# Optimization experiments

Hardware: AMD Instinct MI355X
Metric: run time of the kernel (lower is better)

## Reference

```python
import jax, jax.numpy as jnp
import numpy as np

N_HEADS = 16
DIM = 1024
HEAD_DIM = DIM // N_HEADS

def setup_inputs() -> dict:
    key = jax.random.key(0)
    ks = jax.random.split(key, 5)
    x = jax.random.normal(ks[0], (4, 2048, DIM), dtype=jnp.float32)
    W_attn = jax.random.normal(ks[1], (DIM, 3 * DIM), dtype=jnp.float32) / np.sqrt(DIM)
    b_attn = jnp.zeros((3 * DIM,), dtype=jnp.float32)
    W_proj = jax.random.normal(ks[2], (DIM, DIM), dtype=jnp.float32) / np.sqrt(DIM)
    b_proj = jnp.zeros((DIM,), dtype=jnp.float32)
    return {"x": x, "W_attn": W_attn, "b_attn": b_attn, "W_proj": W_proj, "b_proj": b_proj}

def reference(x, W_attn, b_attn, W_proj, b_proj):
    B, S, D = x.shape
    qkv = x @ W_attn + b_attn                      # [B,S,3D]
    q, k, v = jnp.split(qkv, 3, axis=2)
    def heads(t):
        return t.reshape(B, S, N_HEADS, HEAD_DIM).transpose(0, 2, 1, 3)  # [B,H,S,hd]
    qh, kh, vh = heads(q), heads(k), heads(v)
    scale = 1.0 / np.sqrt(HEAD_DIM).astype(np.float32)
    scores = jnp.einsum('bhqd,bhkd->bhqk', qh, kh) * scale  # [B,H,S,S]
    causal = jnp.tril(jnp.ones((S, S), dtype=bool))
    scores = jnp.where(causal, scores, -jnp.inf)
    probs = jax.nn.softmax(scores, axis=-1)
    ctx = jnp.einsum('bhqk,bhkd->bhqd', probs, vh)           # [B,H,S,hd]
    ctx = ctx.transpose(0, 2, 1, 3).reshape(B, S, D)
    return ctx @ W_proj + b_proj
```

## Files before the change

kernel.cpp:

```cpp
#include <hip/hip_runtime.h>
#include <hip/hip_bf16.h>
#include <stdint.h>

typedef __attribute__((ext_vector_type(4))) float  f32x4a;
typedef __attribute__((ext_vector_type(8))) short  bf16x8s;
typedef __attribute__((ext_vector_type(8))) unsigned short u16x8;

#define QSCALE 0.18033688011112042f

static __device__ __forceinline__ unsigned short f2bf(float f) {
    union { float f; uint32_t u; } v; v.f = f;
    uint32_t u = v.u;
    return (unsigned short)((u + 0x7FFFu + ((u >> 16) & 1u)) >> 16);
}

static __device__ __forceinline__ unsigned int pack2bf(float lo, float hi) {
    __hip_bfloat162 t = __float22bfloat162_rn(make_float2(lo, hi));
    union { __hip_bfloat162 b; unsigned int u; } c; c.b = t;
    return c.u;
}

static __device__ __forceinline__ float exp2a(float x) {
    float r;
    asm("v_exp_f32 %0, %1" : "=v"(r) : "v"(x));
    return r;
}

#define GLL(src, dst)                                                          \
    __builtin_amdgcn_global_load_lds(                                          \
        (const __attribute__((address_space(1))) void*)(src),                  \
        (__attribute__((address_space(3))) void*)(dst), 16, 0, 0)

__global__ __launch_bounds__(256) void k_cvt_bf16(const float* __restrict__ in,
                                                  unsigned short* __restrict__ out, int n8) {
    int i = blockIdx.x * blockDim.x + threadIdx.x;
    if (i >= n8) return;
    const float4* p = (const float4*)(in + (size_t)i * 8);
    float4 a = p[0], b = p[1];
    u16x8 o;
    o[0] = f2bf(a.x); o[1] = f2bf(a.y); o[2] = f2bf(a.z); o[3] = f2bf(a.w);
    o[4] = f2bf(b.x); o[5] = f2bf(b.y); o[6] = f2bf(b.z); o[7] = f2bf(b.w);
    *(u16x8*)(out + (size_t)i * 8) = o;
}

__global__ __launch_bounds__(256) void k_scale_bias(const float* __restrict__ b,
                                                    float* __restrict__ out,
                                                    int n, int nscale, float sc) {
    int i = blockIdx.x * blockDim.x + threadIdx.x;
    if (i >= n) return;
    out[i] = b[i] * (i < nscale ? sc : 1.0f);
}

__global__ __launch_bounds__(256) void k_transpose_w(const float* __restrict__ W,
                                                     unsigned short* __restrict__ Wt,
                                                     int K, int N, float sc, int nscale) {
    __shared__ float tile[64][68];
    int bx = blockIdx.x;
    int ntn = N >> 6;
    int kt = bx / ntn, nt = bx % ntn;
    int t = threadIdx.x;
    int r0 = t >> 4;
    int c4 = (t & 15) << 2;
    for (int i = 0; i < 4; ++i) {
        int k = r0 + i * 16;
        float4 v = *(const float4*)(W + (size_t)(kt * 64 + k) * N + nt * 64 + c4);
        tile[k][c4 + 0] = v.x; tile[k][c4 + 1] = v.y;
        tile[k][c4 + 2] = v.z; tile[k][c4 + 3] = v.w;
    }
    __syncthreads();
    int nl = t >> 2;
    int kc = (t & 3) << 4;
    float s = (nt * 64 + nl < nscale) ? sc : 1.0f;
    unsigned short* dst = Wt + (size_t)(nt * 64 + nl) * K + kt * 64 + kc;
    u16x8 o0, o1;
    for (int i = 0; i < 8; ++i) o0[i] = f2bf(tile[kc + i][nl] * s);
    for (int i = 0; i < 8; ++i) o1[i] = f2bf(tile[kc + 8 + i][nl] * s);
    *(u16x8*)dst = o0;
    *(u16x8*)(dst + 8) = o1;
}

template<int OUT_BF16, int VW>
__global__ __launch_bounds__(512, 4) void k_gemm2b(const unsigned short* __restrict__ A,
                                                   const unsigned short* __restrict__ Bt,
                                                   const float* __restrict__ bias,
                                                   void* __restrict__ Cout,
                                                   unsigned short* __restrict__ vt,
                                                   int M, int N, int K, int ntn) {
    __shared__ __align__(16) unsigned short S[3][12288];
    unsigned short* Sf = &S[0][0];

    int nwg = gridDim.x;
    int bid = blockIdx.x;
    int wg = (bid & 7) * (nwg >> 3) + (bid >> 3);
    int mt = wg / ntn, nt = wg % ntn;
    size_t m0 = (size_t)mt * 128, n0 = (size_t)nt * 256;

    int tid = threadIdx.x;
    int w = tid >> 6, lane = tid & 63;
    int wm = w >> 2, wn = w & 3;
    int l15 = lane & 15, l4 = lane >> 4;

    int srow = tid >> 2;
    int sch = (tid & 3) ^ ((srow >> 1) & 3);
    const unsigned short* Asrc = A  + (m0 + srow) * (size_t)K + sch * 8;
    const unsigned short* Bsrc = Bt + (n0 + srow) * (size_t)K + sch * 8;

#define STG(bufoff, kt)                                                                   \
    do {                                                                                  \
        GLL(Asrc + (size_t)(kt) * 32,                    Sf + (bufoff) + tid * 8);        \
        GLL(Bsrc + (size_t)(kt) * 32,                    Sf + (bufoff) + 4096 + tid * 8); \
        GLL(Bsrc + (size_t)(kt) * 32 + (size_t)128 * K,  Sf + (bufoff) + 8192 + tid * 8); \
    } while (0)

    int ck = (l4 ^ ((l15 >> 1) & 3)) * 8;
    int aoff = (wm * 64 + l15) * 32 + ck;
    int boff = 4096 + (wn * 64 + l15) * 32 + ck;

    f32x4a acc[4][4] = {};

#define BAR() __builtin_amdgcn_s_barrier()

    int NT = K >> 5;

    STG(0, 0);
    STG(12288, 1);
    asm volatile("s_waitcnt vmcnt(3)" ::: "memory");
    __builtin_amdgcn_sched_barrier(0);
    BAR();

    int cb = 0;
    for (int t = 0; t < NT; ++t) {
        int sb = cb + 24576; if (sb >= 36864) sb -= 36864;
        bool more = (t + 2) < NT;
        if (more) STG(sb, t + 2);
        bf16x8s af[4], bf[4];
        #pragma unroll
        for (int q = 0; q < 4; ++q) af[q] = *(const bf16x8s*)(Sf + cb + aoff + q * 512);
        #pragma unroll
        for (int q = 0; q < 4; ++q) bf[q] = *(const bf16x8s*)(Sf + cb + boff + q * 512);
        __builtin_amdgcn_s_setprio(1);
        #pragma unroll
        for (int mf = 0; mf < 4; ++mf)
            #pragma unroll
            for (int nf = 0; nf < 4; ++nf)
                acc[mf][nf] = __builtin_amdgcn_mfma_f32_16x16x32_bf16(af[mf], bf[nf],
                                                                      acc[mf][nf], 0, 0, 0);
        __builtin_amdgcn_s_setprio(0);
        if (more) { asm volatile("s_waitcnt vmcnt(3)" ::: "memory"); }
        else      { asm volatile("s_waitcnt vmcnt(0)" ::: "memory"); }
        __builtin_amdgcn_sched_barrier(0);
        BAR();
        cb += 12288; if (cb >= 36864) cb = 0;
    }

    if (VW && nt >= 8) {
        int b = (int)(m0 >> 11);
        int sb_ = ((int)m0 & 2047) + wm * 64;
        #pragma unroll
        for (int nf = 0; nf < 4; ++nf) {
            int vc = ((int)n0 - 2048) + wn * 64 + nf * 16 + l15;
            int h = vc >> 6, d = vc & 63;
            float bv = bias[2048 + vc];
            unsigned short* vrow = vt + ((size_t)(b * 16 + h) * 64 + d) * 2048;
            #pragma unroll
            for (int mf = 0; mf < 4; ++mf) {
                int s = sb_ + mf * 16 + l4 * 4;
                uint2 pv = make_uint2(pack2bf(acc[mf][nf][0] + bv, acc[mf][nf][1] + bv),
                                      pack2bf(acc[mf][nf][2] + bv, acc[mf][nf][3] + bv));
                *(uint2*)(vrow + s) = pv;
            }
        }
    } else {
        #pragma unroll
        for (int nf = 0; nf < 4; ++nf) {
            int col = (int)n0 + wn * 64 + nf * 16 + l15;
            float bv = bias[col];
            #pragma unroll
            for (int mf = 0; mf < 4; ++mf) {
                int rbase = (int)m0 + wm * 64 + mf * 16 + l4 * 4;
                #pragma unroll
                for (int rr = 0; rr < 4; ++rr) {
                    float v = acc[mf][nf][rr] + bv;
                    if (OUT_BF16)
                        ((unsigned short*)Cout)[(size_t)(rbase + rr) * N + col] = f2bf(v);
                    else
                        ((float*)Cout)[(size_t)(rbase + rr) * N + col] = v;
                }
            }
        }
    }
#undef STG
#undef BAR
}

__global__ __launch_bounds__(256, 2) void k_attn(const unsigned short* __restrict__ qkv,
                                                 const unsigned short* __restrict__ vt,
                                                 unsigned short* __restrict__ ctx) {
    __shared__ unsigned short Ks[3][4096];
    __shared__ unsigned short Vs[3][4096];
    __shared__ unsigned short Pb[4][2048];
    int bx = blockIdx.x;
    int bh = bx & 63;
    int pr = bx >> 6;
    int b = bh >> 4, hd = bh & 15;
    int tid = threadIdx.x;
    int w = tid >> 6, lane = tid & 63;
    int l15 = lane & 15, l4 = lane >> 4;

    const unsigned short* Qb  = qkv + (size_t)b * 2048 * 3072 + hd * 64;
    const unsigned short* Kb  = Qb + 1024;
    const unsigned short* Vtb = vt + (size_t)bh * 64 * 2048;

    int kr0 = tid >> 3, kc0 = tid & 7;
    int kr1 = (tid + 256) >> 3, kc1 = tid & 7;
    const unsigned short* Ksr0 = Kb  + (size_t)kr0 * 3072 + ((kc0 ^ (kr0 & 7)) << 3);
    const unsigned short* Ksr1 = Kb  + (size_t)kr1 * 3072 + ((kc1 ^ (kr1 & 7)) << 3);
    const unsigned short* Vsr0 = Vtb + (size_t)kr0 * 2048 + ((kc0 ^ (kr0 & 7)) << 3);
    const unsigned short* Vsr1 = Vtb + (size_t)kr1 * 2048 + ((kc1 ^ (kr1 & 7)) << 3);
    unsigned short* pbw = &Pb[w][0];

    int psw  = l15 & 7;
    int ph   = (l4 & 1) * 4;
    int pc0  = ((0 + (l4 >> 1)) ^ psw) * 8;
    int pc1  = ((2 + (l4 >> 1)) ^ psw) * 8;
    int pc2  = ((4 + (l4 >> 1)) ^ psw) * 8;
    int pc3  = ((6 + (l4 >> 1)) ^ psw) * 8;
    int pr0  = ((0 + l4) ^ psw) * 8;
    int pr1  = ((4 + l4) ^ psw) * 8;
    int prow0 = l15 * 64;
    int prow1 = (l15 + 16) * 64;

    bf16x8s onesf;
    #pragma unroll
    for (int i = 0; i < 8; ++i) onesf[i] = (short)0x3F80;

#define STAGE(buf, kv0s)                                                                        \
    do {                                                                                        \
        size_t ko_ = (size_t)(kv0s) * 3072;                                                     \
        GLL(Ksr0 + ko_,     &Ks[buf][w * 512]);                                                 \
        GLL(Ksr1 + ko_,     &Ks[buf][2048 + w * 512]);                                          \
        GLL(Vsr0 + (kv0s),  &Vs[buf][w * 512]);                                                 \
        GLL(Vsr1 + (kv0s),  &Vs[buf][2048 + w * 512]);                                          \
    } while (0)

    for (int half = 0; half < 2; ++half) {
        int j = half ? (15 - pr) : pr;
        int q0 = j * 128 + w * 32;
        int qa0 = q0 + l15, qa1 = q0 + 16 + l15;
        bf16x8s qf[2][2];
        {
            const unsigned short* p0 = Qb + (size_t)(q0 + l15) * 3072 + l4 * 8;
            qf[0][0] = *(const bf16x8s*)p0;
            qf[0][1] = *(const bf16x8s*)(p0 + 32);
            const unsigned short* p1 = p0 + (size_t)16 * 3072;
            qf[1][0] = *(const bf16x8s*)p1;
            qf[1][1] = *(const bf16x8s*)(p1 + 32);
        }
        f32x4a o[2][4] = {};
        f32x4a lsum[2] = {};
        const int NSTEPS = 2 * j + 2;

        STAGE(0, 0);
        STAGE(1, 64);
        asm volatile("s_waitcnt vmcnt(4)" ::: "memory");
        __builtin_amdgcn_sched_barrier(0);
        __builtin_amdgcn_s_barrier();

        int s = 0, cur = 0;
        while (true) {
            int kv0 = s << 6;
            bool stg = (s + 2 < NSTEPS);
            int sb = cur + 2; if (sb >= 3) sb -= 3;
            if (stg) STAGE(sb, kv0 + 128);

            if (kv0 <= q0 + 31) {
                const unsigned short* Kbuf = Ks[cur];
                const unsigned short* Vbuf = Vs[cur];

                bf16x8s vf[2][4];
                #pragma unroll
                for (int g = 0; g < 2; ++g)
                    #pragma unroll
                    for (int nf = 0; nf < 4; ++nf) {
                        int rv = nf * 16 + l15;
                        vf[g][nf] = *(const bf16x8s*)(Vbuf + rv * 64 + (((g * 4 + l4) ^ (rv & 7)) << 3));
                    }

                f32x4a z[2][4];
                __builtin_amdgcn_s_setprio(1);
                #pragma unroll
                for (int f = 0; f < 4; ++f) {
                    int rk = f * 16 + l15;
                    bf16x8s ka = *(const bf16x8s*)(Kbuf + rk * 64 + ((l4 ^ psw) << 3));
                    bf16x8s kb = *(const bf16x8s*)(Kbuf + rk * 64 + (((4 + l4) ^ psw) << 3));
                    #pragma unroll
                    for (int g = 0; g < 2; ++g) {
                        f32x4a zz = {0.f, 0.f, 0.f, 0.f};
                        zz = __builtin_amdgcn_mfma_f32_16x16x32_bf16(ka, qf[g][0], zz, 0, 0, 0);
                        zz = __builtin_amdgcn_mfma_f32_16x16x32_bf16(kb, qf[g][1], zz, 0, 0, 0);
                        z[g][f] = zz;
                    }
                }
                __builtin_amdgcn_s_setprio(0);

                if (kv0 + 63 > q0) {
                    #pragma unroll
                    for (int f = 0; f < 4; ++f)
                        #pragma unroll
                        for (int r = 0; r < 4; ++r) {
                            int kvp = kv0 + f * 16 + l4 * 4 + r;
                            if (kvp > qa0) z[0][f][r] = -1e30f;
                            if (kvp > qa1) z[1][f][r] = -1e30f;
                        }
                }

                f32x4a p4[2][4];
                #pragma unroll
                for (int g = 0; g < 2; ++g)
                    #pragma unroll
                    for (int f = 0; f < 4; ++f)
                        #pragma unroll
                        for (int r = 0; r < 4; ++r)
                            p4[g][f][r] = exp2a(z[g][f][r]);

                unsigned int pk[2][8];
                #pragma unroll
                for (int g = 0; g < 2; ++g)
                    #pragma unroll
                    for (int f = 0; f < 4; ++f) {
                        pk[g][2 * f]     = pack2bf(p4[g][f][0], p4[g][f][1]);
                        pk[g][2 * f + 1] = pack2bf(p4[g][f][2], p4[g][f][3]);
                    }

                *(uint2*)(pbw + prow0 + pc0 + ph) = make_uint2(pk[0][0], pk[0][1]);
                *(uint2*)(pbw + prow0 + pc1 + ph) = make_uint2(pk[0][2], pk[0][3]);
                *(uint2*)(pbw + prow0 + pc2 + ph) = make_uint2(pk[0][4], pk[0][5]);
                *(uint2*)(pbw + prow0 + pc3 + ph) = make_uint2(pk[0][6], pk[0][7]);
                *(uint2*)(pbw + prow1 + pc0 + ph) = make_uint2(pk[1][0], pk[1][1]);
                *(uint2*)(pbw + prow1 + pc1 + ph) = make_uint2(pk[1][2], pk[1][3]);
                *(uint2*)(pbw + prow1 + pc2 + ph) = make_uint2(pk[1][4], pk[1][5]);
                *(uint2*)(pbw + prow1 + pc3 + ph) = make_uint2(pk[1][6], pk[1][7]);
                asm volatile("" ::: "memory");
                bf16x8s pa[2][2];
                pa[0][0] = *(const bf16x8s*)(pbw + prow0 + pr0);
                pa[0][1] = *(const bf16x8s*)(pbw + prow0 + pr1);
                pa[1][0] = *(const bf16x8s*)(pbw + prow1 + pr0);
                pa[1][1] = *(const bf16x8s*)(pbw + prow1 + pr1);
                asm volatile("" ::: "memory");

                __builtin_amdgcn_s_setprio(1);
                #pragma unroll
                for (int hh = 0; hh < 2; ++hh)
                    #pragma unroll
                    for (int g = 0; g < 2; ++g) {
                        #pragma unroll
                        for (int nf = 0; nf < 4; ++nf)
                            o[g][nf] = __builtin_amdgcn_mfma_f32_16x16x32_bf16(
                                pa[g][hh], vf[hh][nf], o[g][nf], 0, 0, 0);
                        lsum[g] = __builtin_amdgcn_mfma_f32_16x16x32_bf16(
                            pa[g][hh], onesf, lsum[g], 0, 0, 0);
                    }
                __builtin_amdgcn_s_setprio(0);
            }

            ++s;
            if (s == NSTEPS) break;
            if (stg) { asm volatile("s_waitcnt vmcnt(4)" ::: "memory"); }
            else     { asm volatile("s_waitcnt vmcnt(0)" ::: "memory"); }
            __builtin_amdgcn_sched_barrier(0);
            __builtin_amdgcn_s_barrier();
            cur = cur + 1; if (cur == 3) cur = 0;
        }
        __syncthreads();

        float linv0[4], linv1[4];
        #pragma unroll
        for (int r = 0; r < 4; ++r) {
            linv0[r] = 1.0f / lsum[0][r];
            linv1[r] = 1.0f / lsum[1][r];
        }
        #pragma unroll
        for (int nf = 0; nf < 4; ++nf) {
            int col = hd * 64 + nf * 16 + l15;
            #pragma unroll
            for (int r = 0; r < 4; ++r) {
                int row0 = q0 + l4 * 4 + r;
                ctx[((size_t)b * 2048 + row0) * 1024 + col]      = f2bf(o[0][nf][r] * linv0[r]);
                ctx[((size_t)b * 2048 + row0 + 16) * 1024 + col] = f2bf(o[1][nf][r] * linv1[r]);
            }
        }
    }
#undef STAGE
}

extern "C" void kernel_launch(void* const* d_in, const int* in_sizes, int n_in,
                              void* d_out, int out_size, void* d_ws, size_t ws_size,
                              hipStream_t stream) {
    const float* x      = (const float*)d_in[0];
    const float* W_attn = (const float*)d_in[1];
    const float* b_attn = (const float*)d_in[2];
    const float* W_proj = (const float*)d_in[3];
    const float* b_proj = (const float*)d_in[4];

    char* ws = (char*)d_ws;
    unsigned short* xb  = (unsigned short*)ws; ws += (size_t)8192 * 1024 * 2;
    unsigned short* wta = (unsigned short*)ws; ws += (size_t)3072 * 1024 * 2;
    unsigned short* wtp = (unsigned short*)ws; ws += (size_t)1024 * 1024 * 2;
    unsigned short* qkv = (unsigned short*)ws; ws += (size_t)8192 * 3072 * 2;
    unsigned short* vt  = (unsigned short*)ws; ws += (size_t)64 * 64 * 2048 * 2;
    unsigned short* ctx = (unsigned short*)ws; ws += (size_t)8192 * 1024 * 2;
    float*          sbias = (float*)ws;

    k_cvt_bf16<<<4096, 256, 0, stream>>>(x, xb, 8192 * 1024 / 8);
    k_transpose_w<<<16 * 48, 256, 0, stream>>>(W_attn, wta, 1024, 3072, QSCALE, 1024);
    k_transpose_w<<<16 * 16, 256, 0, stream>>>(W_proj, wtp, 1024, 1024, 1.0f, 0);
    k_scale_bias<<<12, 256, 0, stream>>>(b_attn, sbias, 3072, 1024, QSCALE);
    k_gemm2b<1, 1><<<768, 512, 0, stream>>>(xb, wta, sbias, (void*)qkv, vt, 8192, 3072, 1024, 12);
    k_attn<<<512, 256, 0, stream>>>(qkv, vt, ctx);
    k_gemm2b<0, 0><<<256, 512, 0, stream>>>(ctx, wtp, b_proj, d_out, nullptr, 8192, 1024, 1024, 4);
}
```

Before: 155.7 us.

## Fold bias scaling into GEMM, double-buffer attention KV, drop GEMM setprio

Removes the separate bias-scaling kernel by applying the Q scale to the bias inside the QKV GEMM epilogue, which saves one launch. The attention kernel moves from a 3-stage to a 2-stage K/V LDS ring and raises its launch bound to 3 blocks per SM, cutting LDS use to allow more occupancy. The cost is a full vmcnt(0) wait every step, which shortens prefetch distance. The GEMM main loop also drops its s_setprio hints.

After: 155.4 us. About the same (-0.2%).

```diff
diff --git a/kernel.cpp b/kernel.cpp
--- a/kernel.cpp
+++ b/kernel.cpp
@@ -41,14 +41,6 @@
     o[0] = f2bf(a.x); o[1] = f2bf(a.y); o[2] = f2bf(a.z); o[3] = f2bf(a.w);
     o[4] = f2bf(b.x); o[5] = f2bf(b.y); o[6] = f2bf(b.z); o[7] = f2bf(b.w);
     *(u16x8*)(out + (size_t)i * 8) = o;
-}
-
-__global__ __launch_bounds__(256) void k_scale_bias(const float* __restrict__ b,
-                                                    float* __restrict__ out,
-                                                    int n, int nscale, float sc) {
-    int i = blockIdx.x * blockDim.x + threadIdx.x;
-    if (i >= n) return;
-    out[i] = b[i] * (i < nscale ? sc : 1.0f);
 }
 
 __global__ __launch_bounds__(256) void k_transpose_w(const float* __restrict__ W,
@@ -79,7 +71,7 @@
     *(u16x8*)(dst + 8) = o1;
 }
 
-template<int OUT_BF16, int VW>
+template<int OUT_BF16, int VW, int QS>
 __global__ __launch_bounds__(512, 4) void k_gemm2b(const unsigned short* __restrict__ A,
                                                    const unsigned short* __restrict__ Bt,
                                                    const float* __restrict__ bias,
@@ -138,14 +130,12 @@
         for (int q = 0; q < 4; ++q) af[q] = *(const bf16x8s*)(Sf + cb + aoff + q * 512);
         #pragma unroll
         for (int q = 0; q < 4; ++q) bf[q] = *(const bf16x8s*)(Sf + cb + boff + q * 512);
-        __builtin_amdgcn_s_setprio(1);
         #pragma unroll
         for (int mf = 0; mf < 4; ++mf)
             #pragma unroll
             for (int nf = 0; nf < 4; ++nf)
                 acc[mf][nf] = __builtin_amdgcn_mfma_f32_16x16x32_bf16(af[mf], bf[nf],
                                                                       acc[mf][nf], 0, 0, 0);
-        __builtin_amdgcn_s_setprio(0);
         if (more) { asm volatile("s_waitcnt vmcnt(3)" ::: "memory"); }
         else      { asm volatile("s_waitcnt vmcnt(0)" ::: "memory"); }
         __builtin_amdgcn_sched_barrier(0);
@@ -175,6 +165,7 @@
         for (int nf = 0; nf < 4; ++nf) {
             int col = (int)n0 + wn * 64 + nf * 16 + l15;
             float bv = bias[col];
+            if (QS && col < 1024) bv *= QSCALE;
             #pragma unroll
             for (int mf = 0; mf < 4; ++mf) {
                 int rbase = (int)m0 + wm * 64 + mf * 16 + l4 * 4;
@@ -193,11 +184,11 @@
 #undef BAR
 }
 
-__global__ __launch_bounds__(256, 2) void k_attn(const unsigned short* __restrict__ qkv,
+__global__ __launch_bounds__(256, 3) void k_attn(const unsigned short* __restrict__ qkv,
                                                  const unsigned short* __restrict__ vt,
                                                  unsigned short* __restrict__ ctx) {
-    __shared__ unsigned short Ks[3][4096];
-    __shared__ unsigned short Vs[3][4096];
+    __shared__ unsigned short Ks[2][4096];
+    __shared__ unsigned short Vs[2][4096];
     __shared__ unsigned short Pb[4][2048];
     int bx = blockIdx.x;
     int bh = bx & 63;
@@ -261,17 +252,15 @@
         const int NSTEPS = 2 * j + 2;
 
         STAGE(0, 0);
-        STAGE(1, 64);
-        asm volatile("s_waitcnt vmcnt(4)" ::: "memory");
+        asm volatile("s_waitcnt vmcnt(0)" ::: "memory");
         __builtin_amdgcn_sched_barrier(0);
         __builtin_amdgcn_s_barrier();
 
-        int s = 0, cur = 0;
+        int s = 0;
         while (true) {
+            int cur = s & 1;
             int kv0 = s << 6;
-            bool stg = (s + 2 < NSTEPS);
-            int sb = cur + 2; if (sb >= 3) sb -= 3;
-            if (stg) STAGE(sb, kv0 + 128);
+            if (s + 1 < NSTEPS) STAGE(cur ^ 1, kv0 + 64);
 
             if (kv0 <= q0 + 31) {
                 const unsigned short* Kbuf = Ks[cur];
@@ -365,11 +354,9 @@
 
             ++s;
             if (s == NSTEPS) break;
-            if (stg) { asm volatile("s_waitcnt vmcnt(4)" ::: "memory"); }
-            else     { asm volatile("s_waitcnt vmcnt(0)" ::: "memory"); }
+            asm volatile("s_waitcnt vmcnt(0)" ::: "memory");
             __builtin_amdgcn_sched_barrier(0);
             __builtin_amdgcn_s_barrier();
-            cur = cur + 1; if (cur == 3) cur = 0;
         }
         __syncthreads();
 
@@ -408,14 +395,12 @@
     unsigned short* wtp = (unsigned short*)ws; ws += (size_t)1024 * 1024 * 2;
     unsigned short* qkv = (unsigned short*)ws; ws += (size_t)8192 * 3072 * 2;
     unsigned short* vt  = (unsigned short*)ws; ws += (size_t)64 * 64 * 2048 * 2;
-    unsigned short* ctx = (unsigned short*)ws; ws += (size_t)8192 * 1024 * 2;
-    float*          sbias = (float*)ws;
+    unsigned short* ctx = (unsigned short*)ws;
 
     k_cvt_bf16<<<4096, 256, 0, stream>>>(x, xb, 8192 * 1024 / 8);
     k_transpose_w<<<16 * 48, 256, 0, stream>>>(W_attn, wta, 1024, 3072, QSCALE, 1024);
     k_transpose_w<<<16 * 16, 256, 0, stream>>>(W_proj, wtp, 1024, 1024, 1.0f, 0);
-    k_scale_bias<<<12, 256, 0, stream>>>(b_attn, sbias, 3072, 1024, QSCALE);
-    k_gemm2b<1, 1><<<768, 512, 0, stream>>>(xb, wta, sbias, (void*)qkv, vt, 8192, 3072, 1024, 12);
+    k_gemm2b<1, 1, 1><<<768, 512, 0, stream>>>(xb, wta, b_attn, (void*)qkv, vt, 8192, 3072, 1024, 12);
     k_attn<<<512, 256, 0, stream>>>(qkv, vt, ctx);
-    k_gemm2b<0, 0><<<256, 512, 0, stream>>>(ctx, wtp, b_proj, d_out, nullptr, 8192, 1024, 1024, 4);
-}
+    k_gemm2b<0, 0, 0><<<256, 512, 0, stream>>>(ctx, wtp, b_proj, d_out, nullptr, 8192, 1024, 1024, 4);
+}
```
